# Kernel tuning notes

Hardware: AMD Instinct MI355X
Metric: run time of the kernel (lower is better)

## Reference

```python
import jax, jax.numpy as jnp
import numpy as np

B, C, H, W = 4, 256, 32, 32
N_HEADS, N_GROUPS = 8, 4
HEAD_C = C // N_HEADS            # 32
GROUP_C = C // N_GROUPS          # 64
GROUP_HEADS = N_HEADS // N_GROUPS  # 2
OFFSET_RANGE_FACTOR = 4.0
SCALE = HEAD_C ** -0.5
EPS = 1e-5


def grid_sample(img, grid):
    """Bilinear grid_sample, align_corners=True, zeros padding.
    img: (N, Ch, Hi, Wi); grid: (N, Hg, Wg, 2) with (x, y) in [-1, 1]."""
    N, Ch, Hi, Wi = img.shape
    x = (grid[..., 0] + 1.0) * 0.5 * (Wi - 1)
    y = (grid[..., 1] + 1.0) * 0.5 * (Hi - 1)
    x0 = jnp.floor(x); y0 = jnp.floor(y)
    x1 = x0 + 1.0; y1 = y0 + 1.0
    wx1 = x - x0; wx0 = 1.0 - wx1
    wy1 = y - y0; wy0 = 1.0 - wy1
    img_flat = img.reshape(N, Ch, Hi * Wi)

    def corner(xi, yi, w):
        valid = (xi >= 0) & (xi <= Wi - 1) & (yi >= 0) & (yi <= Hi - 1)
        xc = jnp.clip(xi, 0, Wi - 1).astype(jnp.int32)
        yc = jnp.clip(yi, 0, Hi - 1).astype(jnp.int32)
        idx = yc * Wi + xc  # (N, Hg, Wg)
        vals = jax.vmap(lambda im, ix: im[:, ix])(img_flat, idx)  # (N, Ch, Hg, Wg)
        return vals * (w * valid)[:, None, :, :]

    return (corner(x0, y0, wx0 * wy0) + corner(x1, y0, wx1 * wy0)
            + corner(x0, y1, wx0 * wy1) + corner(x1, y1, wx1 * wy1))


def setup_inputs() -> dict:
    key = jax.random.key(0)
    ks = jax.random.split(key, 12)
    s = C ** -0.5
    return {
        "q_feat": jax.random.normal(ks[0], (B, C, H, W), jnp.float32),
        "kv_feat": jax.random.normal(ks[1], (B, C, H, W), jnp.float32),
        "Wq": jax.random.normal(ks[2], (C, C), jnp.float32) * s,
        "bq": jnp.zeros((C,), jnp.float32),
        "Wk": jax.random.normal(ks[3], (C, C), jnp.float32) * s,
        "bk": jnp.zeros((C,), jnp.float32),
        "Wv": jax.random.normal(ks[4], (C, C), jnp.float32) * s,
        "bv": jnp.zeros((C,), jnp.float32),
        "Wo": jax.random.normal(ks[5], (C, C), jnp.float32) * s,
        "bo": jnp.zeros((C,), jnp.float32),
        "off_dw_w": jax.random.normal(ks[6], (GROUP_C, 1, 3, 3), jnp.float32) / 3.0,
        "off_dw_b": jnp.zeros((GROUP_C,), jnp.float32),
        "off_ln_w": jnp.ones((GROUP_C,), jnp.float32),
        "off_ln_b": jnp.zeros((GROUP_C,), jnp.float32),
        "off_pw_w": jax.random.normal(ks[7], (2, GROUP_C), jnp.float32) * GROUP_C ** -0.5,
        "rpe_table": jax.random.normal(ks[8], (N_HEADS, 2 * H - 1, 2 * W - 1), jnp.float32) * 0.01,
    }


def reference(q_feat, kv_feat, Wq, bq, Wk, bk, Wv, bv, Wo, bo,
              off_dw_w, off_dw_b, off_ln_w, off_ln_b, off_pw_w, rpe_table):
    Bg = B * N_GROUPS
    n = H * W
    # q projection (1x1 conv)
    q = jnp.einsum('oi,bihw->bohw', Wq, q_feat) + bq[:, None, None]
    # offset network on grouped q
    q_off = q.reshape(Bg, GROUP_C, H, W)
    x = jax.lax.conv_general_dilated(q_off, off_dw_w, (1, 1), ((1, 1), (1, 1)),
                                     feature_group_count=GROUP_C,
                                     dimension_numbers=('NCHW', 'OIHW', 'NCHW'))
    x = x + off_dw_b[:, None, None]
    mu = x.mean(1, keepdims=True)
    var = x.var(1, keepdims=True)
    x = (x - mu) / jnp.sqrt(var + EPS) * off_ln_w[:, None, None] + off_ln_b[:, None, None]
    x = jax.nn.gelu(x, approximate=False)
    offset = jnp.einsum('oc,bchw->bohw', off_pw_w, x)  # (Bg, 2, H, W), (y, x)
    off_range = jnp.array([1.0 / (H - 1), 1.0 / (W - 1)], jnp.float32).reshape(1, 2, 1, 1)
    offset = jnp.tanh(offset) * off_range * OFFSET_RANGE_FACTOR
    offset = offset.transpose(0, 2, 3, 1)  # (Bg, H, W, 2)
    # reference points in [-1, 1]
    ref_y = (jnp.linspace(0.5, H - 0.5, H) / (H - 1.0)) * 2.0 - 1.0
    ref_x = (jnp.linspace(0.5, W - 0.5, W) / (W - 1.0)) * 2.0 - 1.0
    ref = jnp.stack(jnp.meshgrid(ref_y, ref_x, indexing='ij'), -1)  # (H, W, 2)
    pos = offset + ref[None]  # (Bg, H, W, 2), (y, x), no clamp (offset_range_factor >= 0)
    # deformable sampling of kv features
    kv_g = kv_feat.reshape(Bg, GROUP_C, H, W)
    x_sampled = grid_sample(kv_g, pos[..., ::-1]).reshape(B, C, n)
    k = jnp.einsum('oi,bin->bon', Wk, x_sampled) + bk[:, None]
    v = jnp.einsum('oi,bin->bon', Wv, x_sampled) + bv[:, None]
    qf = q.reshape(B, N_HEADS, HEAD_C, n)
    kf = k.reshape(B, N_HEADS, HEAD_C, n)
    vf = v.reshape(B, N_HEADS, HEAD_C, n)
    attn = jnp.einsum('bhcm,bhcn->bhmn', qf, kf) * SCALE
    # relative-position bias via bilinear sampling of rpe table
    gy = (jnp.arange(H, dtype=jnp.float32) / (H - 1.0)) * 2.0 - 1.0
    gx = (jnp.arange(W, dtype=jnp.float32) / (W - 1.0)) * 2.0 - 1.0
    q_grid = jnp.stack(jnp.meshgrid(gy, gx, indexing='ij'), -1).reshape(n, 2)
    pos_flat = pos.reshape(Bg, n, 2)
    disp = (q_grid[None, :, None, :] - pos_flat[:, None, :, :]) * 0.5  # (Bg, m, n, 2)
    rpe = jnp.broadcast_to(
        rpe_table.reshape(1, N_GROUPS, GROUP_HEADS, 2 * H - 1, 2 * W - 1),
        (B, N_GROUPS, GROUP_HEADS, 2 * H - 1, 2 * W - 1)
    ).reshape(Bg, GROUP_HEADS, 2 * H - 1, 2 * W - 1)
    bias = grid_sample(rpe, disp[..., ::-1])  # (Bg, GROUP_HEADS, m, n)
    attn = attn + bias.reshape(B, N_HEADS, n, n)
    attn = jax.nn.softmax(attn, axis=-1)
    out = jnp.einsum('bhmn,bhcn->bhcm', attn, vf).reshape(B, C, H, W)
    out = jnp.einsum('oi,bihw->bohw', Wo, out) + bo[:, None, None]
    return out
```

## Files before the change

### kernel.cpp

```cpp
#include <hip/hip_runtime.h>
#include <hip/hip_bf16.h>
#include <math.h>
#include <stdint.h>

#define BB 4
#define CC 256
#define HH 32
#define WW 32
#define NPIX 1024
#define NHEADS 8
#define NGROUPS 4
#define HEADC 32
#define GROUPC 64
#define BG 16
#define RPE_N 3969
#define SCALE_QK 0.17677669529663687f
#define LN_EPS 1e-5f

#define W_Q   0
#define W_POS 1048576
#define W_XS  1081344
#define W_KT  2129920
#define W_VV  2654208
#define W_AO  3178496
#define W_RPE 4227072
#define W_WSP 4264608

#define RPE_PACKED 4692
#define PLANE (1u << 20)

using frag  = __attribute__((ext_vector_type(8))) short;
using f32x4 = __attribute__((ext_vector_type(4))) float;

struct InPtrs { const void* p[16]; };

__device__ __forceinline__ float tof(float x){ return x; }
__device__ __forceinline__ float tof(__hip_bfloat16 x){ return __bfloat162float(x); }
__device__ __forceinline__ bool is_f32(const void* lnw) {
  return *(const unsigned int*)lnw == 0x3F800000u;
}
__device__ __forceinline__ float ldm(const void* p, size_t i, bool f32m) {
  return f32m ? ((const float*)p)[i] : __bfloat162float(((const __hip_bfloat16*)p)[i]);
}
__device__ __forceinline__ float lof(uint32_t g){ return __uint_as_float(g << 16); }
__device__ __forceinline__ float hif(uint32_t g){ return __uint_as_float(g & 0xffff0000u); }
__device__ __forceinline__ void split16(float v, unsigned short* ph, unsigned short* pl) {
  __hip_bfloat16 h = __float2bfloat16(v);
  *ph = *(unsigned short*)&h;
  __hip_bfloat16 l = __float2bfloat16(v - __bfloat162float(h));
  *pl = *(unsigned short*)&l;
}

__global__ __launch_bounds__(512, 2)
void prep_kernel(InPtrs ip, uint32_t* __restrict__ rpeg,
                 unsigned short* __restrict__ wsp,
                 unsigned short* __restrict__ qf) {
  bool f32m = is_f32(ip.p[12]);
  int blk = blockIdx.x;
  int tid = threadIdx.x;
  if (blk < 8) {
    int h = blk;
    const size_t rbase = (size_t)h * RPE_N;
    uint32_t* dst = rpeg + (size_t)h * RPE_PACKED;
    for (int i = tid; i < 68 * 69; i += 512) {
      int r = i / 69, c = i - r * 69;
      int y = r - 3, x = c - 3;
      bool yv = (y >= 0) & (y < 63);
      float va = (yv & (x >= 0) & (x < 63)) ? ldm(ip.p[15], rbase + y * 63 + x, f32m) : 0.0f;
      float vb2 = (yv & (x >= -1) & (x < 62)) ? ldm(ip.p[15], rbase + y * 63 + x + 1, f32m) : 0.0f;
      __hip_bfloat16 ha = __float2bfloat16(va), hb = __float2bfloat16(vb2);
      dst[i] = (uint32_t)*(unsigned short*)&ha | ((uint32_t)*(unsigned short*)&hb << 16);
    }
  } else if (blk < 72) {
    int wb = blk - 8;
    const void* srcs[4] = { ip.p[2], ip.p[4], ip.p[6], ip.p[8] };
    int idx0 = wb * 4096 + tid * 8;
    int m = idx0 >> 16, e0 = idx0 & 65535;
    const void* src = srcs[m];
    unsigned short* hi = wsp + (size_t)m * 131072;
    unsigned short* lo = hi + 65536;
    #pragma unroll
    for (int j = 0; j < 8; ++j) {
      float w = ldm(src, e0 + j, f32m);
      split16(w, &hi[e0 + j], &lo[e0 + j]);
    }
  } else {
    int wb2 = blk - 72;
    int e0 = wb2 * 4096 + tid * 8;
    #pragma unroll
    for (int j = 0; j < 8; ++j) {
      float w = ldm(ip.p[0], e0 + j, f32m);
      split16(w, &qf[e0 + j], &qf[PLANE + e0 + j]);
    }
  }
}

template<int TM>
__device__ __forceinline__ void gemm_body(const unsigned short* __restrict__ xh,
    const unsigned short* __restrict__ xl,
    const unsigned short* __restrict__ wsp, int b, int o0, int mb,
    short* Bs, f32x4* acc) {
  const int tid = threadIdx.x;
  const int wave = tid >> 6, lane = tid & 63, quad = lane >> 4, l15 = lane & 15;
  const int og = wave & 3, mh = wave >> 2;
  const int MS = TM >> 5;
  const int NE = TM >> 4;

  size_t gbase[NE];
  int lbase[NE];
  #pragma unroll
  for (int it = 0; it < NE; ++it) {
    int i = tid + 512 * it;
    int mm = i & (TM - 1), kk = i / TM;
    gbase[it] = ((size_t)(b * CC + kk)) * NPIX + mb + mm;
    lbase[it] = mm * 72 + ((((kk >> 3) ^ (mm & 3))) << 4) + (kk & 7);
  }

  unsigned short vh[NE], vl[NE];
  #pragma unroll
  for (int it = 0; it < NE; ++it) {
    vh[it] = xh[gbase[it]];
    vl[it] = xl[gbase[it]];
  }

  for (int s = 0; s < 8; ++s) {
    short* buf = Bs + (s & 1) * (TM * 72);
    #pragma unroll
    for (int it = 0; it < NE; ++it) {
      buf[lbase[it]] = (short)vh[it];
      buf[lbase[it] + 8] = (short)vl[it];
    }
    if (s < 7) {
      size_t koff = (size_t)(s + 1) * 32 * NPIX;
      #pragma unroll
      for (int it = 0; it < NE; ++it) {
        vh[it] = xh[gbase[it] + koff];
        vl[it] = xl[gbase[it] + koff];
      }
    }
    const int k0 = s * 32;
    size_t wofs = (size_t)(o0 + og * 16 + l15) * CC + k0 + quad * 8;
    frag wh = *(const frag*)(wsp + wofs);
    frag wl = *(const frag*)(wsp + 65536 + wofs);
    __syncthreads();
    #pragma unroll
    for (int ms = 0; ms < MS; ++ms) {
      int ml = mh * (TM >> 1) + ms * 16 + l15;
      const short* bp = buf + ml * 72 + ((quad ^ (ml & 3)) << 4);
      frag bh = *(const frag*)bp;
      frag bl = *(const frag*)(bp + 8);
      acc[ms] = __builtin_amdgcn_mfma_f32_16x16x32_bf16(wh, bh, acc[ms], 0, 0, 0);
      acc[ms] = __builtin_amdgcn_mfma_f32_16x16x32_bf16(wh, bl, acc[ms], 0, 0, 0);
      acc[ms] = __builtin_amdgcn_mfma_f32_16x16x32_bf16(wl, bh, acc[ms], 0, 0, 0);
    }
  }
}

__global__ __launch_bounds__(512, 2)
void qproj_kernel(InPtrs ip, const unsigned short* __restrict__ qf,
                  const unsigned short* __restrict__ wsp,
                  float* __restrict__ q) {
  __shared__ __align__(16) short Bs[2 * 32 * 72];
  bool f32m = is_f32(ip.p[12]);
  int mb = blockIdx.x * 32, o0 = blockIdx.y * 64, b = blockIdx.z;
  int tid = threadIdx.x;
  int wave = tid >> 6, lane = tid & 63, quad = lane >> 4, l15 = lane & 15;
  f32x4 acc[1] = {{0.f,0.f,0.f,0.f}};
  gemm_body<32>(qf, qf + PLANE, wsp, b, o0, mb, Bs, acc);
  int og = wave & 3, mh = wave >> 2;
  int od = o0 + og * 16 + quad * 4;
  float bv[4];
  #pragma unroll
  for (int r = 0; r < 4; ++r) bv[r] = ldm(ip.p[3], od + r, f32m);
  int m = mb + mh * 16 + l15;
  #pragma unroll
  for (int r = 0; r < 4; ++r)
    q[(size_t)(b * CC + od + r) * NPIX + m] = acc[0][r] + bv[r];
}

__global__ __launch_bounds__(512, 2)
void kvproj_kernel(InPtrs ip, const unsigned short* __restrict__ xsp,
                   const unsigned short* __restrict__ wspal,
                   __hip_bfloat16* __restrict__ kT, __hip_bfloat16* __restrict__ vbf) {
  __shared__ __align__(16) char arena[2 * 64 * 72 * 2];
  bool f32m = is_f32(ip.p[12]);
  int mt = blockIdx.x, ot = blockIdx.y, b = blockIdx.z;
  int mb = mt * 64;
  bool isV = (ot >= 4);
  int o0 = (ot & 3) * 64;
  const unsigned short* wsp = wspal + (size_t)(isV ? 2 : 1) * 131072;
  const void* braw = isV ? ip.p[7] : ip.p[5];
  int tid = threadIdx.x;
  int wave = tid >> 6, lane = tid & 63, quad = lane >> 4, l15 = lane & 15;
  f32x4 acc[2] = {{0.f,0.f,0.f,0.f},{0.f,0.f,0.f,0.f}};
  gemm_body<64>(xsp, xsp + PLANE, wsp, b, o0, mb, (short*)arena, acc);
  int og = wave & 3, mh = wave >> 2;
  int od = o0 + og * 16 + quad * 4;
  float bv[4];
  #pragma unroll
  for (int r = 0; r < 4; ++r) bv[r] = ldm(braw, od + r, f32m);
  if (isV) {
    #pragma unroll
    for (int ms = 0; ms < 2; ++ms) {
      int m = mb + mh * 32 + ms * 16 + l15;
      #pragma unroll
      for (int r = 0; r < 4; ++r)
        vbf[(size_t)(b * CC + od + r) * NPIX + m] = __float2bfloat16(acc[ms][r] + bv[r]);
    }
  } else {
    __syncthreads();
    float* Ds = (float*)arena;
    #pragma unroll
    for (int ms = 0; ms < 2; ++ms) {
      int ml = mh * 32 + ms * 16 + l15;
      #pragma unroll
      for (int r = 0; r < 4; ++r)
        Ds[(og * 16 + quad * 4 + r) * 65 + ml] = acc[ms][r] + bv[r];
    }
    __syncthreads();
    int ot4 = ot & 3;
    {
      int q2 = tid;
      int m = q2 >> 3, cc = q2 & 7;
      __hip_bfloat16 t8[8];
      #pragma unroll
      for (int j = 0; j < 8; ++j)
        t8[j] = __float2bfloat16(Ds[(cc * 8 + j) * 65 + m]);
      int h = ot4 * 2 + (cc >> 2);
      size_t addr = ((size_t)(b * NHEADS + h) * NPIX + mb + m) * HEADC + (cc & 3) * 8;
      *(uint4*)((short*)kT + addr) = *(const uint4*)t8;
    }
  }
}

__global__ __launch_bounds__(512, 2)
void oproj_kernel(InPtrs ip, const unsigned short* __restrict__ aop,
                  const unsigned short* __restrict__ wsp, void* __restrict__ out) {
  __shared__ __align__(16) short Bs[2 * 32 * 72];
  bool f32m = is_f32(ip.p[12]);
  int mb = blockIdx.x * 32, o0 = blockIdx.y * 64, b = blockIdx.z;
  int tid = threadIdx.x;
  int wave = tid >> 6, lane = tid & 63, quad = lane >> 4, l15 = lane & 15;
  f32x4 acc[1] = {{0.f,0.f,0.f,0.f}};
  gemm_body<32>(aop, aop + PLANE, wsp, b, o0, mb, Bs, acc);
  int og = wave & 3, mh = wave >> 2;
  int od = o0 + og * 16 + quad * 4;
  float bv[4];
  #pragma unroll
  for (int r = 0; r < 4; ++r) bv[r] = ldm(ip.p[9], od + r, f32m);
  int m = mb + mh * 16 + l15;
  #pragma unroll
  for (int r = 0; r < 4; ++r) {
    float val = acc[0][r] + bv[r];
    size_t idx = (size_t)(b * CC + od + r) * NPIX + m;
    if (f32m) ((float*)out)[idx] = val;
    else      ((__hip_bfloat16*)out)[idx] = __float2bfloat16(val);
  }
}

template<typename T>
__device__ __forceinline__ float tap4(const T* __restrict__ img,
                                      int x0, int y0,
                                      float wx0, float wx1, float wy0, float wy1) {
  bool xv0 = (x0 >= 0) & (x0 < WW);
  bool xv1 = (x0 >= -1) & (x0 < WW - 1);
  bool yv0 = (y0 >= 0) & (y0 < HH);
  bool yv1 = (y0 >= -1) & (y0 < HH - 1);
  float acc = 0.0f;
  if (xv0 & yv0) acc += wx0 * wy0 * tof(img[y0 * WW + x0]);
  if (xv1 & yv0) acc += wx1 * wy0 * tof(img[y0 * WW + x0 + 1]);
  if (xv0 & yv1) acc += wx0 * wy1 * tof(img[(y0 + 1) * WW + x0]);
  if (xv1 & yv1) acc += wx1 * wy1 * tof(img[(y0 + 1) * WW + x0 + 1]);
  return acc;
}

__global__ __launch_bounds__(512, 2)
void offsample_kernel(InPtrs ip, const float* __restrict__ q,
                      float* __restrict__ pos, unsigned short* __restrict__ xsp) {
  __shared__ float qs[96][65];
  __shared__ float posl[64];
  bool f32m = is_f32(ip.p[12]);
  int blk = blockIdx.x;
  int hh = blk & 31, bg = blk >> 5;
  int b = bg >> 2, g = bg & 3;
  int tid = threadIdx.x;
  const float* qg = q + (size_t)(b * CC + g * GROUPC) * NPIX;
  #pragma unroll
  for (int k = 0; k < 12; ++k) {
    int idx = tid + 512 * k;
    int ww = idx & 31, c = (idx >> 5) & 63, r3 = idx >> 11;
    int yy = hh - 1 + r3;
    float v = (yy >= 0 && yy < HH) ? qg[(size_t)c * NPIX + yy * WW + ww] : 0.0f;
    qs[r3 * 32 + ww][c] = v;
  }
  __syncthreads();
  {
    int wave = tid >> 6, c = tid & 63;
    float wdw[9];
    #pragma unroll
    for (int j = 0; j < 9; ++j) wdw[j] = ldm(ip.p[10], c * 9 + j, f32m);
    float bdw = ldm(ip.p[11], c, f32m);
    float lnw = ldm(ip.p[12], c, f32m), lnb = ldm(ip.p[13], c, f32m);
    float pwy = ldm(ip.p[14], c, f32m), pwx = ldm(ip.p[14], GROUPC + c, f32m);

    float xv[4];
    #pragma unroll
    for (int p = 0; p < 4; ++p) {
      int ww = wave * 4 + p;
      float x = bdw;
      #pragma unroll
      for (int dy = 0; dy < 3; ++dy)
        #pragma unroll
        for (int dx = 0; dx < 3; ++dx) {
          int xx = ww + dx - 1;
          if (xx >= 0 && xx < WW) x += wdw[dy * 3 + dx] * qs[dy * 32 + xx][c];
        }
      xv[p] = x;
    }
    float sA[4], s2A[4];
    #pragma unroll
    for (int p = 0; p < 4; ++p) { sA[p] = xv[p]; s2A[p] = xv[p] * xv[p]; }
    #pragma unroll
    for (int off = 32; off > 0; off >>= 1)
      #pragma unroll
      for (int p = 0; p < 4; ++p) {
        sA[p]  += __shfl_xor(sA[p],  off);
        s2A[p] += __shfl_xor(s2A[p], off);
      }
    float oyA[4], oxA[4];
    #pragma unroll
    for (int p = 0; p < 4; ++p) {
      float mu  = sA[p] * (1.0f / 64.0f);
      float var = s2A[p] * (1.0f / 64.0f) - mu * mu;
      float xn = (xv[p] - mu) * (1.0f / sqrtf(var + LN_EPS)) * lnw + lnb;
      float ge = 0.5f * xn * (1.0f + erff(xn * 0.70710678118654752f));
      oyA[p] = pwy * ge; oxA[p] = pwx * ge;
    }
    #pragma unroll
    for (int off = 32; off > 0; off >>= 1)
      #pragma unroll
      for (int p = 0; p < 4; ++p) {
        oyA[p] += __shfl_xor(oyA[p], off);
        oxA[p] += __shfl_xor(oxA[p], off);
      }
    if (c == 0) {
      #pragma unroll
      for (int p = 0; p < 4; ++p) {
        int ww = wave * 4 + p;
        float fy = tanhf(oyA[p]) * (4.0f / 31.0f);
        float fx = tanhf(oxA[p]) * (4.0f / 31.0f);
        float ry = ((0.5f + (float)hh) / 31.0f) * 2.0f - 1.0f;
        float rx = ((0.5f + (float)ww) / 31.0f) * 2.0f - 1.0f;
        float py = fy + ry, px = fx + rx;
        int m = hh * 32 + ww;
        pos[((size_t)bg * NPIX + m) * 2 + 0] = py;
        pos[((size_t)bg * NPIX + m) * 2 + 1] = px;
        posl[ww * 2 + 0] = py;
        posl[ww * 2 + 1] = px;
      }
    }
  }
  __syncthreads();
  #pragma unroll
  for (int k = 0; k < 4; ++k) {
    int s = tid + 512 * k;
    int ww = s & 31, c = (s >> 5) & 63;
    float py = posl[ww * 2 + 0], px = posl[ww * 2 + 1];
    float xi = (px + 1.0f) * 15.5f, yi = (py + 1.0f) * 15.5f;
    float x0f = floorf(xi), y0f = floorf(yi);
    float wx1 = xi - x0f, wx0 = 1.0f - wx1;
    float wy1 = yi - y0f, wy0 = 1.0f - wy1;
    int x0 = (int)x0f, y0 = (int)y0f;
    size_t img_off = (size_t)(b * CC + g * GROUPC + c) * NPIX;
    float acc;
    if (f32m) acc = tap4((const float*)ip.p[1] + img_off, x0, y0, wx0, wx1, wy0, wy1);
    else      acc = tap4((const __hip_bfloat16*)ip.p[1] + img_off, x0, y0, wx0, wx1, wy0, wy1);
    size_t oidx = img_off + hh * 32 + ww;
    split16(acc, &xsp[oidx], &xsp[PLANE + oidx]);
  }
}

__global__ __launch_bounds__(512, 4)
void attn_mfma_kernel(InPtrs ip, const uint32_t* __restrict__ rpeg,
                      const float* __restrict__ q,
                      const __hip_bfloat16* __restrict__ kT,
                      const __hip_bfloat16* __restrict__ vbf,
                      const float* __restrict__ pos,
                      unsigned short* __restrict__ aop) {
  __shared__ __align__(16) uint32_t Du[RPE_PACKED];
  __shared__ __align__(16) __hip_bfloat16 Pw[8][16][72];
  __shared__ __align__(16) __hip_bfloat16 qA[16][40];
  __shared__ float redmax[8 * 16];
  __shared__ float redsum[8 * 16];

  int bh = blockIdx.x;
  int b = bh >> 3, h = bh & 7;
  int m0 = blockIdx.y * 16;
  int tid = threadIdx.x;
  int bg = b * 4 + (h >> 1);

  size_t slice = (size_t)(b * CC + h * HEADC) * NPIX;
  const short* kTb = (const short*)kT + (size_t)bh * NPIX * HEADC;
  const short* vb = (const short*)vbf + slice;
  const float* qb = q + slice;
  const float* posb = pos + (size_t)bg * NPIX * 2;

  {
    const uint4* src = (const uint4*)(rpeg + (size_t)h * RPE_PACKED);
    uint4* dst = (uint4*)Du;
    for (int i = tid; i < 1173; i += 512) dst[i] = src[i];
  }
  {
    int r = tid & 15, c = tid >> 4;
    qA[r][c] = __float2bfloat16(qb[(size_t)c * NPIX + m0 + r] * SCALE_QK);
  }
  __syncthreads();

  int wave = tid >> 6, lane = tid & 63;
  int quad = lane >> 4, l15 = lane & 15;
  int nbase = wave * 128;

  frag aq = *(const frag*)&qA[l15][quad * 8];
  float ybase = 31.0f + 15.5f * ((float)(m0 >> 5) * (2.0f / 31.0f) - 1.0f);
  float xbase0 = 31.0f + 15.5f * ((float)(m0 & 31) * (2.0f / 31.0f) - 1.0f);

  float pm[4], ps[4];
  f32x4 acc0 = {0.f,0.f,0.f,0.f}, acc1 = {0.f,0.f,0.f,0.f};
  #pragma unroll
  for (int reg = 0; reg < 4; ++reg) { pm[reg] = -1e30f; ps[reg] = 0.0f; }

  #pragma unroll
  for (int half = 0; half < 2; ++half) {
    int hbase = nbase + half * 64;
    float sreg[4][4];
    #pragma unroll
    for (int t8 = 0; t8 < 4; ++t8) {
      int n = hbase + t8 * 16 + l15;
      frag bk = *(const frag*)(kTb + (size_t)n * HEADC + quad * 8);
      f32x4 d = __builtin_amdgcn_mfma_f32_16x16x32_bf16(aq, bk, (f32x4){0.f,0.f,0.f,0.f}, 0, 0, 0);
      float2 pp = *(const float2*)(posb + 2 * n);
      float yi = ybase - 15.5f * pp.x;
      float y0f = floorf(yi);
      float wy1 = yi - y0f, wy0 = 1.0f - wy1;
      float xi0 = xbase0 - 15.5f * pp.y;
      float x0f = floorf(xi0);
      float wx1 = xi0 - x0f, wx0 = 1.0f - wx1;
      int row = (int)y0f + 3;
      int col = (int)x0f + 3 + quad * 4;
      const uint32_t* Dp = Du + row * 69 + col;
      uint32_t g0 = Dp[0],  g1 = Dp[2],  g2 = Dp[4];
      uint32_t h0 = Dp[69], h1 = Dp[71], h2 = Dp[73];
      float u[5];
      u[0] = wy0 * lof(g0) + wy1 * lof(h0);
      u[1] = wy0 * hif(g0) + wy1 * hif(h0);
      u[2] = wy0 * lof(g1) + wy1 * lof(h1);
      u[3] = wy0 * hif(g1) + wy1 * hif(h1);
      u[4] = wy0 * lof(g2) + wy1 * lof(h2);
      #pragma unroll
      for (int reg = 0; reg < 4; ++reg)
        sreg[t8][reg] = d[reg] + wx0 * u[reg] + wx1 * u[reg + 1];
    }
    #pragma unroll
    for (int reg = 0; reg < 4; ++reg) {
      float m = fmaxf(fmaxf(sreg[0][reg], sreg[1][reg]),
                      fmaxf(sreg[2][reg], sreg[3][reg]));
      m = fmaxf(m, __shfl_xor(m, 1));
      m = fmaxf(m, __shfl_xor(m, 2));
      m = fmaxf(m, __shfl_xor(m, 4));
      m = fmaxf(m, __shfl_xor(m, 8));
      float newm = fmaxf(pm[reg], m);
      float sc = __expf(pm[reg] - newm);
      pm[reg] = newm;
      ps[reg] *= sc;
      acc0[reg] *= sc;
      acc1[reg] *= sc;
    }
    #pragma unroll
    for (int t8 = 0; t8 < 4; ++t8) {
      #pragma unroll
      for (int reg = 0; reg < 4; ++reg) {
        float p = __expf(sreg[t8][reg] - pm[reg]);
        Pw[wave][quad * 4 + reg][t8 * 16 + l15] = __float2bfloat16(p);
        ps[reg] += p;
      }
    }
    #pragma unroll
    for (int ks = 0; ks < 2; ++ks) {
      int koff = hbase + ks * 32 + quad * 8;
      frag ap = *(const frag*)&Pw[wave][l15][ks * 32 + quad * 8];
      frag bv0 = *(const frag*)(vb + (size_t)l15 * NPIX + koff);
      frag bv1 = *(const frag*)(vb + (size_t)(16 + l15) * NPIX + koff);
      acc0 = __builtin_amdgcn_mfma_f32_16x16x32_bf16(ap, bv0, acc0, 0, 0, 0);
      acc1 = __builtin_amdgcn_mfma_f32_16x16x32_bf16(ap, bv1, acc1, 0, 0, 0);
    }
  }

  #pragma unroll
  for (int reg = 0; reg < 4; ++reg) {
    ps[reg] += __shfl_xor(ps[reg], 1);
    ps[reg] += __shfl_xor(ps[reg], 2);
    ps[reg] += __shfl_xor(ps[reg], 4);
    ps[reg] += __shfl_xor(ps[reg], 8);
  }
  if (l15 == 0) {
    #pragma unroll
    for (int reg = 0; reg < 4; ++reg) {
      redmax[wave * 16 + quad * 4 + reg] = pm[reg];
      redsum[wave * 16 + quad * 4 + reg] = ps[reg];
    }
  }
  __syncthreads();

  float* part = (float*)&Pw[0][0][0];
  {
    int e0 = (0 * 16 + l15) * 16 + quad * 4;
    int e1 = (1 * 16 + l15) * 16 + quad * 4;
    #pragma unroll
    for (int reg = 0; reg < 4; ++reg) {
      part[wave * 512 + e0 + reg] = acc0[reg];
      part[wave * 512 + e1 + reg] = acc1[reg];
    }
  }
  __syncthreads();

  {
    int c = tid >> 4, r = tid & 15;
    float M = -1e30f;
    #pragma unroll
    for (int w2 = 0; w2 < 8; ++w2) M = fmaxf(M, redmax[w2 * 16 + r]);
    float num = 0.0f, den = 0.0f;
    #pragma unroll
    for (int w2 = 0; w2 < 8; ++w2) {
      float sc = __expf(redmax[w2 * 16 + r] - M);
      num += part[w2 * 512 + tid] * sc;
      den += redsum[w2 * 16 + r] * sc;
    }
    size_t oidx = slice + (size_t)c * NPIX + m0 + r;
    split16(num / den, &aop[oidx], &aop[PLANE + oidx]);
  }
}

extern "C" void kernel_launch(void* const* d_in, const int* in_sizes, int n_in,
                              void* d_out, int out_size, void* d_ws, size_t ws_size,
                              hipStream_t stream) {
  float* ws  = (float*)d_ws;
  float* q   = ws + W_Q;
  float* pos = ws + W_POS;
  unsigned short* xsp = (unsigned short*)(ws + W_XS);
  __hip_bfloat16* kT  = (__hip_bfloat16*)(ws + W_KT);
  __hip_bfloat16* vbf = (__hip_bfloat16*)(ws + W_VV);
  unsigned short* aop = (unsigned short*)(ws + W_AO);
  uint32_t* rpeg = (uint32_t*)(ws + W_RPE);
  unsigned short* wsp = (unsigned short*)(ws + W_WSP);
  unsigned short* qf = (unsigned short*)(ws + W_KT);

  InPtrs ip;
  for (int i = 0; i < 16; ++i) ip.p[i] = d_in[i];

  prep_kernel<<<328, 512, 0, stream>>>(ip, rpeg, wsp, qf);
  qproj_kernel<<<dim3(32, 4, 4), 512, 0, stream>>>(ip, qf, wsp, q);
  offsample_kernel<<<BG * 32, 512, 0, stream>>>(ip, q, pos, xsp);
  kvproj_kernel<<<dim3(16, 8, 4), 512, 0, stream>>>(ip, xsp, wsp, kT, vbf);
  attn_mfma_kernel<<<dim3(32, 64), 512, 0, stream>>>(ip, rpeg, q, kT, vbf, pos, aop);
  oproj_kernel<<<dim3(32, 4, 4), 512, 0, stream>>>(ip, aop, wsp + (size_t)3 * 131072, d_out);
}
```

Baseline: 181.4 us.

## Fuse prep, Q-proj, offset sampling and KV-proj into one persistent kernel with grid barriers

Replaces four separate kernel launches (prep, q projection, offset/sampling, kv projection) with a single 512-block persistent kernel that separates the stages with a software grid barrier built from atomics in workspace. The aim is to remove launch gaps and per-kernel tail drain between these short stages. In exchange it adds a memset launch and barrier spin overhead. It also relies on all 512 blocks being co-resident, which __launch_bounds__(512,2) and 256 CUs should allow; otherwise it deadlocks.

```diff
diff --git a/kernel.cpp b/kernel.cpp
--- a/kernel.cpp
+++ b/kernel.cpp
@@ -25,9 +25,11 @@
 #define W_AO  3178496
 #define W_RPE 4227072
 #define W_WSP 4264608
+#define W_SYNC 4600000
 
 #define RPE_PACKED 4692
 #define PLANE (1u << 20)
+#define FUSED_NB 512
 
 using frag  = __attribute__((ext_vector_type(8))) short;
 using f32x4 = __attribute__((ext_vector_type(4))) float;
@@ -51,48 +53,26 @@
   *pl = *(unsigned short*)&l;
 }
 
-__global__ __launch_bounds__(512, 2)
-void prep_kernel(InPtrs ip, uint32_t* __restrict__ rpeg,
-                 unsigned short* __restrict__ wsp,
-                 unsigned short* __restrict__ qf) {
-  bool f32m = is_f32(ip.p[12]);
-  int blk = blockIdx.x;
-  int tid = threadIdx.x;
-  if (blk < 8) {
-    int h = blk;
-    const size_t rbase = (size_t)h * RPE_N;
-    uint32_t* dst = rpeg + (size_t)h * RPE_PACKED;
-    for (int i = tid; i < 68 * 69; i += 512) {
-      int r = i / 69, c = i - r * 69;
-      int y = r - 3, x = c - 3;
-      bool yv = (y >= 0) & (y < 63);
-      float va = (yv & (x >= 0) & (x < 63)) ? ldm(ip.p[15], rbase + y * 63 + x, f32m) : 0.0f;
-      float vb2 = (yv & (x >= -1) & (x < 62)) ? ldm(ip.p[15], rbase + y * 63 + x + 1, f32m) : 0.0f;
-      __hip_bfloat16 ha = __float2bfloat16(va), hb = __float2bfloat16(vb2);
-      dst[i] = (uint32_t)*(unsigned short*)&ha | ((uint32_t)*(unsigned short*)&hb << 16);
-    }
-  } else if (blk < 72) {
-    int wb = blk - 8;
-    const void* srcs[4] = { ip.p[2], ip.p[4], ip.p[6], ip.p[8] };
-    int idx0 = wb * 4096 + tid * 8;
-    int m = idx0 >> 16, e0 = idx0 & 65535;
-    const void* src = srcs[m];
-    unsigned short* hi = wsp + (size_t)m * 131072;
-    unsigned short* lo = hi + 65536;
-    #pragma unroll
-    for (int j = 0; j < 8; ++j) {
-      float w = ldm(src, e0 + j, f32m);
-      split16(w, &hi[e0 + j], &lo[e0 + j]);
-    }
-  } else {
-    int wb2 = blk - 72;
-    int e0 = wb2 * 4096 + tid * 8;
-    #pragma unroll
-    for (int j = 0; j < 8; ++j) {
-      float w = ldm(ip.p[0], e0 + j, f32m);
-      split16(w, &qf[e0 + j], &qf[PLANE + e0 + j]);
-    }
-  }
+__device__ __forceinline__ void gbar(unsigned* __restrict__ cnt,
+                                     unsigned* __restrict__ gen) {
+  __syncthreads();
+  if (threadIdx.x == 0) {
+    __threadfence();
+    unsigned g = __hip_atomic_load(gen, __ATOMIC_RELAXED, __HIP_MEMORY_SCOPE_AGENT);
+    unsigned a = __hip_atomic_fetch_add(cnt, 1u, __ATOMIC_ACQ_REL, __HIP_MEMORY_SCOPE_AGENT);
+    if (a == FUSED_NB - 1) {
+      __hip_atomic_store(cnt, 0u, __ATOMIC_RELAXED, __HIP_MEMORY_SCOPE_AGENT);
+      __hip_atomic_store(gen, g + 1u, __ATOMIC_RELEASE, __HIP_MEMORY_SCOPE_AGENT);
+    } else {
+      unsigned cur;
+      do {
+        __builtin_amdgcn_s_sleep(2);
+        cur = __hip_atomic_load(gen, __ATOMIC_ACQUIRE, __HIP_MEMORY_SCOPE_AGENT);
+      } while (cur == g);
+    }
+    __threadfence();
+  }
+  __syncthreads();
 }
 
 template<int TM>
@@ -153,108 +133,6 @@
       acc[ms] = __builtin_amdgcn_mfma_f32_16x16x32_bf16(wh, bl, acc[ms], 0, 0, 0);
       acc[ms] = __builtin_amdgcn_mfma_f32_16x16x32_bf16(wl, bh, acc[ms], 0, 0, 0);
     }
-  }
-}
-
-__global__ __launch_bounds__(512, 2)
-void qproj_kernel(InPtrs ip, const unsigned short* __restrict__ qf,
-                  const unsigned short* __restrict__ wsp,
-                  float* __restrict__ q) {
-  __shared__ __align__(16) short Bs[2 * 32 * 72];
-  bool f32m = is_f32(ip.p[12]);
-  int mb = blockIdx.x * 32, o0 = blockIdx.y * 64, b = blockIdx.z;
-  int tid = threadIdx.x;
-  int wave = tid >> 6, lane = tid & 63, quad = lane >> 4, l15 = lane & 15;
-  f32x4 acc[1] = {{0.f,0.f,0.f,0.f}};
-  gemm_body<32>(qf, qf + PLANE, wsp, b, o0, mb, Bs, acc);
-  int og = wave & 3, mh = wave >> 2;
-  int od = o0 + og * 16 + quad * 4;
-  float bv[4];
-  #pragma unroll
-  for (int r = 0; r < 4; ++r) bv[r] = ldm(ip.p[3], od + r, f32m);
-  int m = mb + mh * 16 + l15;
-  #pragma unroll
-  for (int r = 0; r < 4; ++r)
-    q[(size_t)(b * CC + od + r) * NPIX + m] = acc[0][r] + bv[r];
-}
-
-__global__ __launch_bounds__(512, 2)
-void kvproj_kernel(InPtrs ip, const unsigned short* __restrict__ xsp,
-                   const unsigned short* __restrict__ wspal,
-                   __hip_bfloat16* __restrict__ kT, __hip_bfloat16* __restrict__ vbf) {
-  __shared__ __align__(16) char arena[2 * 64 * 72 * 2];
-  bool f32m = is_f32(ip.p[12]);
-  int mt = blockIdx.x, ot = blockIdx.y, b = blockIdx.z;
-  int mb = mt * 64;
-  bool isV = (ot >= 4);
-  int o0 = (ot & 3) * 64;
-  const unsigned short* wsp = wspal + (size_t)(isV ? 2 : 1) * 131072;
-  const void* braw = isV ? ip.p[7] : ip.p[5];
-  int tid = threadIdx.x;
-  int wave = tid >> 6, lane = tid & 63, quad = lane >> 4, l15 = lane & 15;
-  f32x4 acc[2] = {{0.f,0.f,0.f,0.f},{0.f,0.f,0.f,0.f}};
-  gemm_body<64>(xsp, xsp + PLANE, wsp, b, o0, mb, (short*)arena, acc);
-  int og = wave & 3, mh = wave >> 2;
-  int od = o0 + og * 16 + quad * 4;
-  float bv[4];
-  #pragma unroll
-  for (int r = 0; r < 4; ++r) bv[r] = ldm(braw, od + r, f32m);
-  if (isV) {
-    #pragma unroll
-    for (int ms = 0; ms < 2; ++ms) {
-      int m = mb + mh * 32 + ms * 16 + l15;
-      #pragma unroll
-      for (int r = 0; r < 4; ++r)
-        vbf[(size_t)(b * CC + od + r) * NPIX + m] = __float2bfloat16(acc[ms][r] + bv[r]);
-    }
-  } else {
-    __syncthreads();
-    float* Ds = (float*)arena;
-    #pragma unroll
-    for (int ms = 0; ms < 2; ++ms) {
-      int ml = mh * 32 + ms * 16 + l15;
-      #pragma unroll
-      for (int r = 0; r < 4; ++r)
-        Ds[(og * 16 + quad * 4 + r) * 65 + ml] = acc[ms][r] + bv[r];
-    }
-    __syncthreads();
-    int ot4 = ot & 3;
-    {
-      int q2 = tid;
-      int m = q2 >> 3, cc = q2 & 7;
-      __hip_bfloat16 t8[8];
-      #pragma unroll
-      for (int j = 0; j < 8; ++j)
-        t8[j] = __float2bfloat16(Ds[(cc * 8 + j) * 65 + m]);
-      int h = ot4 * 2 + (cc >> 2);
-      size_t addr = ((size_t)(b * NHEADS + h) * NPIX + mb + m) * HEADC + (cc & 3) * 8;
-      *(uint4*)((short*)kT + addr) = *(const uint4*)t8;
-    }
-  }
-}
-
-__global__ __launch_bounds__(512, 2)
-void oproj_kernel(InPtrs ip, const unsigned short* __restrict__ aop,
-                  const unsigned short* __restrict__ wsp, void* __restrict__ out) {
-  __shared__ __align__(16) short Bs[2 * 32 * 72];
-  bool f32m = is_f32(ip.p[12]);
-  int mb = blockIdx.x * 32, o0 = blockIdx.y * 64, b = blockIdx.z;
-  int tid = threadIdx.x;
-  int wave = tid >> 6, lane = tid & 63, quad = lane >> 4, l15 = lane & 15;
-  f32x4 acc[1] = {{0.f,0.f,0.f,0.f}};
-  gemm_body<32>(aop, aop + PLANE, wsp, b, o0, mb, Bs, acc);
-  int og = wave & 3, mh = wave >> 2;
-  int od = o0 + og * 16 + quad * 4;
-  float bv[4];
-  #pragma unroll
-  for (int r = 0; r < 4; ++r) bv[r] = ldm(ip.p[9], od + r, f32m);
-  int m = mb + mh * 16 + l15;
-  #pragma unroll
-  for (int r = 0; r < 4; ++r) {
-    float val = acc[0][r] + bv[r];
-    size_t idx = (size_t)(b * CC + od + r) * NPIX + m;
-    if (f32m) ((float*)out)[idx] = val;
-    else      ((__hip_bfloat16*)out)[idx] = __float2bfloat16(val);
   }
 }
 
@@ -275,108 +153,252 @@
 }
 
 __global__ __launch_bounds__(512, 2)
-void offsample_kernel(InPtrs ip, const float* __restrict__ q,
-                      float* __restrict__ pos, unsigned short* __restrict__ xsp) {
-  __shared__ float qs[96][65];
-  __shared__ float posl[64];
+void fused_aux_kernel(InPtrs ip, unsigned* __restrict__ syncp,
+                      uint32_t* __restrict__ rpeg,
+                      unsigned short* __restrict__ wsp,
+                      unsigned short* __restrict__ qf,
+                      float* __restrict__ q,
+                      float* __restrict__ pos,
+                      unsigned short* __restrict__ xsp,
+                      __hip_bfloat16* __restrict__ kT,
+                      __hip_bfloat16* __restrict__ vbf) {
+  __shared__ __align__(16) char smem[25344];
+  unsigned* cnt = syncp;
+  unsigned* gen = syncp + 16;
   bool f32m = is_f32(ip.p[12]);
-  int blk = blockIdx.x;
-  int hh = blk & 31, bg = blk >> 5;
-  int b = bg >> 2, g = bg & 3;
-  int tid = threadIdx.x;
-  const float* qg = q + (size_t)(b * CC + g * GROUPC) * NPIX;
-  #pragma unroll
-  for (int k = 0; k < 12; ++k) {
-    int idx = tid + 512 * k;
-    int ww = idx & 31, c = (idx >> 5) & 63, r3 = idx >> 11;
-    int yy = hh - 1 + r3;
-    float v = (yy >= 0 && yy < HH) ? qg[(size_t)c * NPIX + yy * WW + ww] : 0.0f;
-    qs[r3 * 32 + ww][c] = v;
-  }
-  __syncthreads();
-  {
-    int wave = tid >> 6, c = tid & 63;
-    float wdw[9];
-    #pragma unroll
-    for (int j = 0; j < 9; ++j) wdw[j] = ldm(ip.p[10], c * 9 + j, f32m);
-    float bdw = ldm(ip.p[11], c, f32m);
-    float lnw = ldm(ip.p[12], c, f32m), lnb = ldm(ip.p[13], c, f32m);
-    float pwy = ldm(ip.p[14], c, f32m), pwx = ldm(ip.p[14], GROUPC + c, f32m);
-
-    float xv[4];
-    #pragma unroll
-    for (int p = 0; p < 4; ++p) {
-      int ww = wave * 4 + p;
-      float x = bdw;
-      #pragma unroll
-      for (int dy = 0; dy < 3; ++dy)
-        #pragma unroll
-        for (int dx = 0; dx < 3; ++dx) {
-          int xx = ww + dx - 1;
-          if (xx >= 0 && xx < WW) x += wdw[dy * 3 + dx] * qs[dy * 32 + xx][c];
-        }
-      xv[p] = x;
-    }
-    float sA[4], s2A[4];
-    #pragma unroll
-    for (int p = 0; p < 4; ++p) { sA[p] = xv[p]; s2A[p] = xv[p] * xv[p]; }
-    #pragma unroll
-    for (int off = 32; off > 0; off >>= 1)
-      #pragma unroll
-      for (int p = 0; p < 4; ++p) {
-        sA[p]  += __shfl_xor(sA[p],  off);
-        s2A[p] += __shfl_xor(s2A[p], off);
-      }
-    float oyA[4], oxA[4];
-    #pragma unroll
-    for (int p = 0; p < 4; ++p) {
-      float mu  = sA[p] * (1.0f / 64.0f);
-      float var = s2A[p] * (1.0f / 64.0f) - mu * mu;
-      float xn = (xv[p] - mu) * (1.0f / sqrtf(var + LN_EPS)) * lnw + lnb;
-      float ge = 0.5f * xn * (1.0f + erff(xn * 0.70710678118654752f));
-      oyA[p] = pwy * ge; oxA[p] = pwx * ge;
-    }
-    #pragma unroll
-    for (int off = 32; off > 0; off >>= 1)
-      #pragma unroll
-      for (int p = 0; p < 4; ++p) {
-        oyA[p] += __shfl_xor(oyA[p], off);
-        oxA[p] += __shfl_xor(oxA[p], off);
-      }
-    if (c == 0) {
+  const int blk = blockIdx.x;
+  const int tid = threadIdx.x;
+
+  if (blk < 8) {
+    int h = blk;
+    const size_t rbase = (size_t)h * RPE_N;
+    uint32_t* dst = rpeg + (size_t)h * RPE_PACKED;
+    for (int i = tid; i < 68 * 69; i += 512) {
+      int r = i / 69, c = i - r * 69;
+      int y = r - 3, x = c - 3;
+      bool yv = (y >= 0) & (y < 63);
+      float va = (yv & (x >= 0) & (x < 63)) ? ldm(ip.p[15], rbase + y * 63 + x, f32m) : 0.0f;
+      float vb2 = (yv & (x >= -1) & (x < 62)) ? ldm(ip.p[15], rbase + y * 63 + x + 1, f32m) : 0.0f;
+      __hip_bfloat16 ha = __float2bfloat16(va), hb = __float2bfloat16(vb2);
+      dst[i] = (uint32_t)*(unsigned short*)&ha | ((uint32_t)*(unsigned short*)&hb << 16);
+    }
+  } else if (blk < 72) {
+    int wb = blk - 8;
+    const void* srcs[4] = { ip.p[2], ip.p[4], ip.p[6], ip.p[8] };
+    int idx0 = wb * 4096 + tid * 8;
+    int m = idx0 >> 16, e0 = idx0 & 65535;
+    const void* src = srcs[m];
+    unsigned short* hi = wsp + (size_t)m * 131072;
+    unsigned short* lo = hi + 65536;
+    #pragma unroll
+    for (int j = 0; j < 8; ++j) {
+      float w = ldm(src, e0 + j, f32m);
+      split16(w, &hi[e0 + j], &lo[e0 + j]);
+    }
+  } else if (blk < 328) {
+    int wb2 = blk - 72;
+    int e0 = wb2 * 4096 + tid * 8;
+    #pragma unroll
+    for (int j = 0; j < 8; ++j) {
+      float w = ldm(ip.p[0], e0 + j, f32m);
+      split16(w, &qf[e0 + j], &qf[PLANE + e0 + j]);
+    }
+  }
+  gbar(cnt, gen);
+
+  {
+    int mt = blk & 31, ot = (blk >> 5) & 3, b = blk >> 7;
+    int mb = mt * 32, o0 = ot * 64;
+    short* Bs = (short*)smem;
+    int wave = tid >> 6, lane = tid & 63, quad = lane >> 4, l15 = lane & 15;
+    f32x4 acc[1] = {{0.f,0.f,0.f,0.f}};
+    gemm_body<32>(qf, qf + PLANE, wsp, b, o0, mb, Bs, acc);
+    int og = wave & 3, mh = wave >> 2;
+    int od = o0 + og * 16 + quad * 4;
+    float bv[4];
+    #pragma unroll
+    for (int r = 0; r < 4; ++r) bv[r] = ldm(ip.p[3], od + r, f32m);
+    int m = mb + mh * 16 + l15;
+    #pragma unroll
+    for (int r = 0; r < 4; ++r)
+      q[(size_t)(b * CC + od + r) * NPIX + m] = acc[0][r] + bv[r];
+  }
+  gbar(cnt, gen);
+
+  {
+    float (*qs)[65] = (float(*)[65])smem;
+    float* posl = (float*)(smem + 24960);
+    int hh = blk & 31, bg = blk >> 5;
+    int b = bg >> 2, g = bg & 3;
+    const float* qg = q + (size_t)(b * CC + g * GROUPC) * NPIX;
+    #pragma unroll
+    for (int k = 0; k < 12; ++k) {
+      int idx = tid + 512 * k;
+      int ww = idx & 31, c = (idx >> 5) & 63, r3 = idx >> 11;
+      int yy = hh - 1 + r3;
+      float v = (yy >= 0 && yy < HH) ? qg[(size_t)c * NPIX + yy * WW + ww] : 0.0f;
+      qs[r3 * 32 + ww][c] = v;
+    }
+    __syncthreads();
+    {
+      int wave = tid >> 6, c = tid & 63;
+      float wdw[9];
+      #pragma unroll
+      for (int j = 0; j < 9; ++j) wdw[j] = ldm(ip.p[10], c * 9 + j, f32m);
+      float bdw = ldm(ip.p[11], c, f32m);
+      float lnw = ldm(ip.p[12], c, f32m), lnb = ldm(ip.p[13], c, f32m);
+      float pwy = ldm(ip.p[14], c, f32m), pwx = ldm(ip.p[14], GROUPC + c, f32m);
+
+      float xv[4];
       #pragma unroll
       for (int p = 0; p < 4; ++p) {
         int ww = wave * 4 + p;
-        float fy = tanhf(oyA[p]) * (4.0f / 31.0f);
-        float fx = tanhf(oxA[p]) * (4.0f / 31.0f);
-        float ry = ((0.5f + (float)hh) / 31.0f) * 2.0f - 1.0f;
-        float rx = ((0.5f + (float)ww) / 31.0f) * 2.0f - 1.0f;
-        float py = fy + ry, px = fx + rx;
-        int m = hh * 32 + ww;
-        pos[((size_t)bg * NPIX + m) * 2 + 0] = py;
-        pos[((size_t)bg * NPIX + m) * 2 + 1] = px;
-        posl[ww * 2 + 0] = py;
-        posl[ww * 2 + 1] = px;
-      }
-    }
-  }
-  __syncthreads();
-  #pragma unroll
-  for (int k = 0; k < 4; ++k) {
-    int s = tid + 512 * k;
-    int ww = s & 31, c = (s >> 5) & 63;
-    float py = posl[ww * 2 + 0], px = posl[ww * 2 + 1];
-    float xi = (px + 1.0f) * 15.5f, yi = (py + 1.0f) * 15.5f;
-    float x0f = floorf(xi), y0f = floorf(yi);
-    float wx1 = xi - x0f, wx0 = 1.0f - wx1;
-    float wy1 = yi - y0f, wy0 = 1.0f - wy1;
-    int x0 = (int)x0f, y0 = (int)y0f;
-    size_t img_off = (size_t)(b * CC + g * GROUPC + c) * NPIX;
-    float acc;
-    if (f32m) acc = tap4((const float*)ip.p[1] + img_off, x0, y0, wx0, wx1, wy0, wy1);
-    else      acc = tap4((const __hip_bfloat16*)ip.p[1] + img_off, x0, y0, wx0, wx1, wy0, wy1);
-    size_t oidx = img_off + hh * 32 + ww;
-    split16(acc, &xsp[oidx], &xsp[PLANE + oidx]);
+        float x = bdw;
+        #pragma unroll
+        for (int dy = 0; dy < 3; ++dy)
+          #pragma unroll
+          for (int dx = 0; dx < 3; ++dx) {
+            int xx = ww + dx - 1;
+            if (xx >= 0 && xx < WW) x += wdw[dy * 3 + dx] * qs[dy * 32 + xx][c];
+          }
+        xv[p] = x;
+      }
+      float sA[4], s2A[4];
+      #pragma unroll
+      for (int p = 0; p < 4; ++p) { sA[p] = xv[p]; s2A[p] = xv[p] * xv[p]; }
+      #pragma unroll
+      for (int off = 32; off > 0; off >>= 1)
+        #pragma unroll
+        for (int p = 0; p < 4; ++p) {
+          sA[p]  += __shfl_xor(sA[p],  off);
+          s2A[p] += __shfl_xor(s2A[p], off);
+        }
+      float oyA[4], oxA[4];
+      #pragma unroll
+      for (int p = 0; p < 4; ++p) {
+        float mu  = sA[p] * (1.0f / 64.0f);
+        float var = s2A[p] * (1.0f / 64.0f) - mu * mu;
+        float xn = (xv[p] - mu) * (1.0f / sqrtf(var + LN_EPS)) * lnw + lnb;
+        float ge = 0.5f * xn * (1.0f + erff(xn * 0.70710678118654752f));
+        oyA[p] = pwy * ge; oxA[p] = pwx * ge;
+      }
+      #pragma unroll
+      for (int off = 32; off > 0; off >>= 1)
+        #pragma unroll
+        for (int p = 0; p < 4; ++p) {
+          oyA[p] += __shfl_xor(oyA[p], off);
+          oxA[p] += __shfl_xor(oxA[p], off);
+        }
+      if (c == 0) {
+        #pragma unroll
+        for (int p = 0; p < 4; ++p) {
+          int ww = wave * 4 + p;
+          float fy = tanhf(oyA[p]) * (4.0f / 31.0f);
+          float fx = tanhf(oxA[p]) * (4.0f / 31.0f);
+          float ry = ((0.5f + (float)hh) / 31.0f) * 2.0f - 1.0f;
+          float rx = ((0.5f + (float)ww) / 31.0f) * 2.0f - 1.0f;
+          float py = fy + ry, px = fx + rx;
+          int m = hh * 32 + ww;
+          pos[((size_t)bg * NPIX + m) * 2 + 0] = py;
+          pos[((size_t)bg * NPIX + m) * 2 + 1] = px;
+          posl[ww * 2 + 0] = py;
+          posl[ww * 2 + 1] = px;
+        }
+      }
+    }
+    __syncthreads();
+    #pragma unroll
+    for (int k = 0; k < 4; ++k) {
+      int s = tid + 512 * k;
+      int ww = s & 31, c = (s >> 5) & 63;
+      float py = posl[ww * 2 + 0], px = posl[ww * 2 + 1];
+      float xi = (px + 1.0f) * 15.5f, yi = (py + 1.0f) * 15.5f;
+      float x0f = floorf(xi), y0f = floorf(yi);
+      float wx1 = xi - x0f, wx0 = 1.0f - wx1;
+      float wy1 = yi - y0f, wy0 = 1.0f - wy1;
+      int x0 = (int)x0f, y0 = (int)y0f;
+      size_t img_off = (size_t)(b * CC + g * GROUPC + c) * NPIX;
+      float acc;
+      if (f32m) acc = tap4((const float*)ip.p[1] + img_off, x0, y0, wx0, wx1, wy0, wy1);
+      else      acc = tap4((const __hip_bfloat16*)ip.p[1] + img_off, x0, y0, wx0, wx1, wy0, wy1);
+      size_t oidx = img_off + hh * 32 + ww;
+      split16(acc, &xsp[oidx], &xsp[PLANE + oidx]);
+    }
+  }
+  gbar(cnt, gen);
+
+  {
+    char* arena = smem;
+    int mt = blk & 15, ot = (blk >> 4) & 7, b = blk >> 7;
+    int mb = mt * 64;
+    bool isV = (ot >= 4);
+    int o0 = (ot & 3) * 64;
+    const unsigned short* wspk = wsp + (size_t)(isV ? 2 : 1) * 131072;
+    const void* braw = isV ? ip.p[7] : ip.p[5];
+    int wave = tid >> 6, lane = tid & 63, quad = lane >> 4, l15 = lane & 15;
+    f32x4 acc[2] = {{0.f,0.f,0.f,0.f},{0.f,0.f,0.f,0.f}};
+    gemm_body<64>(xsp, xsp + PLANE, wspk, b, o0, mb, (short*)arena, acc);
+    int og = wave & 3, mh = wave >> 2;
+    int od = o0 + og * 16 + quad * 4;
+    float bv[4];
+    #pragma unroll
+    for (int r = 0; r < 4; ++r) bv[r] = ldm(braw, od + r, f32m);
+    if (isV) {
+      #pragma unroll
+      for (int ms = 0; ms < 2; ++ms) {
+        int m = mb + mh * 32 + ms * 16 + l15;
+        #pragma unroll
+        for (int r = 0; r < 4; ++r)
+          vbf[(size_t)(b * CC + od + r) * NPIX + m] = __float2bfloat16(acc[ms][r] + bv[r]);
+      }
+    } else {
+      __syncthreads();
+      float* Ds = (float*)arena;
+      #pragma unroll
+      for (int ms = 0; ms < 2; ++ms) {
+        int ml = mh * 32 + ms * 16 + l15;
+        #pragma unroll
+        for (int r = 0; r < 4; ++r)
+          Ds[(og * 16 + quad * 4 + r) * 65 + ml] = acc[ms][r] + bv[r];
+      }
+      __syncthreads();
+      int ot4 = ot & 3;
+      {
+        int m = tid >> 3, cc = tid & 7;
+        __hip_bfloat16 t8[8];
+        #pragma unroll
+        for (int j = 0; j < 8; ++j)
+          t8[j] = __float2bfloat16(Ds[(cc * 8 + j) * 65 + m]);
+        int h = ot4 * 2 + (cc >> 2);
+        size_t addr = ((size_t)(b * NHEADS + h) * NPIX + mb + m) * HEADC + (cc & 3) * 8;
+        *(uint4*)((short*)kT + addr) = *(const uint4*)t8;
+      }
+    }
+  }
+}
+
+__global__ __launch_bounds__(512, 2)
+void oproj_kernel(InPtrs ip, const unsigned short* __restrict__ aop,
+                  const unsigned short* __restrict__ wsp, void* __restrict__ out) {
+  __shared__ __align__(16) short Bs[2 * 32 * 72];
+  bool f32m = is_f32(ip.p[12]);
+  int mb = blockIdx.x * 32, o0 = blockIdx.y * 64, b = blockIdx.z;
+  int tid = threadIdx.x;
+  int wave = tid >> 6, lane = tid & 63, quad = lane >> 4, l15 = lane & 15;
+  f32x4 acc[1] = {{0.f,0.f,0.f,0.f}};
+  gemm_body<32>(aop, aop + PLANE, wsp, b, o0, mb, Bs, acc);
+  int og = wave & 3, mh = wave >> 2;
+  int od = o0 + og * 16 + quad * 4;
+  float bv[4];
+  #pragma unroll
+  for (int r = 0; r < 4; ++r) bv[r] = ldm(ip.p[9], od + r, f32m);
+  int m = mb + mh * 16 + l15;
+  #pragma unroll
+  for (int r = 0; r < 4; ++r) {
+    float val = acc[0][r] + bv[r];
+    size_t idx = (size_t)(b * CC + od + r) * NPIX + m;
+    if (f32m) ((float*)out)[idx] = val;
+    else      ((__hip_bfloat16*)out)[idx] = __float2bfloat16(val);
   }
 }
 
@@ -552,15 +574,15 @@
   unsigned short* aop = (unsigned short*)(ws + W_AO);
   uint32_t* rpeg = (uint32_t*)(ws + W_RPE);
   unsigned short* wsp = (unsigned short*)(ws + W_WSP);
+  unsigned* syncp = (unsigned*)(ws + W_SYNC);
   unsigned short* qf = (unsigned short*)(ws + W_KT);
 
   InPtrs ip;
   for (int i = 0; i < 16; ++i) ip.p[i] = d_in[i];
 
-  prep_kernel<<<328, 512, 0, stream>>>(ip, rpeg, wsp, qf);
-  qproj_kernel<<<dim3(32, 4, 4), 512, 0, stream>>>(ip, qf, wsp, q);
-  offsample_kernel<<<BG * 32, 512, 0, stream>>>(ip, q, pos, xsp);
-  kvproj_kernel<<<dim3(16, 8, 4), 512, 0, stream>>>(ip, xsp, wsp, kT, vbf);
+  hipMemsetAsync(syncp, 0, 256, stream);
+  fused_aux_kernel<<<FUSED_NB, 512, 0, stream>>>(ip, syncp, rpeg, wsp, qf,
+                                                 q, pos, xsp, kT, vbf);
   attn_mfma_kernel<<<dim3(32, 64), 512, 0, stream>>>(ip, rpeg, q, kT, vbf, pos, aop);
   oproj_kernel<<<dim3(32, 4, 4), 512, 0, stream>>>(ip, aop, wsp + (size_t)3 * 131072, d_out);
 }
```

Measured after the change: 521.5 us. 2.87x slower.
